# Kernel tuning notes

Hardware: AMD Instinct MI355X
Metric: run time of the kernel (lower is better)

## Reference

```python
import jax, jax.numpy as jnp
import numpy as np

B, T, NU, NX, NY = 16, 4096, 64, 256, 32

def setup_inputs() -> dict:
    key = jax.random.key(0)
    ks = jax.random.split(key, 7)
    s = 1.0 / np.sqrt(NX)
    return {
        "inputs": jax.random.normal(ks[0], (B, T, NU), dtype=jnp.float32),
        "h0": jax.random.uniform(ks[1], (B, NX), dtype=jnp.float32),
        "H_w": jax.random.normal(ks[2], (NX, NX), dtype=jnp.float32) * s,
        "H_b": jax.random.normal(ks[3], (NX,), dtype=jnp.float32) * s,
        "K_w": jax.random.normal(ks[4], (NX, NU), dtype=jnp.float32) * (1.0 / np.sqrt(NU)),
        "E_inv": jnp.eye(NX, dtype=jnp.float32),  # E = I in the original module
        "out_w": jax.random.normal(ks[5], (NY, NX), dtype=jnp.float32) * s,
        "out_b": jax.random.normal(ks[6], (NY,), dtype=jnp.float32) * s,
    }

def reference(inputs, h0, H_w, H_b, K_w, E_inv, out_w, out_b):
    # Precompute input projections for all steps: [B, T, NX]
    Ku = jnp.einsum("btu,xu->btx", inputs, K_w)
    seq_len = inputs.shape[1]

    def step(ht, ku_t):
        xt = ht @ H_w.T + H_b + ku_t          # Linear(H) + Linear(K)
        ht_new = jax.nn.relu(xt) @ E_inv      # nonlinearity then fixed matrix
        return ht_new, ht_new

    # loop runs seq_len - 1 times; states start with h0
    _, hs = jax.lax.scan(step, h0, jnp.swapaxes(Ku[:, : seq_len - 1, :], 0, 1))
    states = jnp.concatenate([h0[:, None, :], jnp.swapaxes(hs, 0, 1)], axis=1)  # [B, T, NX]
    yest = states @ out_w.T + out_b  # [B, T, NY]
    return (yest, states)
```

## Files before the change

### kernel.cpp

```cpp
#include <hip/hip_runtime.h>

#define Bsz 16
#define Tl  4096
#define NUc 64
#define NXc 256
#define NYc 32

template <int CTRL>
__device__ __forceinline__ float dpp_add(float x) {
    int y = __builtin_amdgcn_update_dpp(0, __float_as_int(x), CTRL, 0xf, 0xf, true);
    return x + __int_as_float(y);
}
__device__ __forceinline__ float quad_reduce4(float x) {
    x = dpp_add<0x4E>(x);
    x = dpp_add<0xB1>(x);
    return x;
}
__device__ __forceinline__ float row_reduce16(float x) {
    x = dpp_add<0x128>(x);
    x = dpp_add<0x124>(x);
    x = dpp_add<0x4E>(x);
    x = dpp_add<0xB1>(x);
    return x;
}

#define KEEPF(x) asm volatile("" : "+v"(x))

#define DECLW(T,P) \
    float T##P##_0,T##P##_1,T##P##_2,T##P##_3,T##P##_4,T##P##_5,T##P##_6,T##P##_7, \
          T##P##_8,T##P##_9,T##P##_10,T##P##_11,T##P##_12,T##P##_13,T##P##_14,T##P##_15
#define LOADW(T,P,RP) { \
    const float* wr_ = (RP) + 16*P; \
    float4 a_=*(const float4*)(wr_+0), b_=*(const float4*)(wr_+4); \
    float4 c_=*(const float4*)(wr_+8), d_=*(const float4*)(wr_+12); \
    T##P##_0 =a_.x; T##P##_1 =a_.y; T##P##_2 =a_.z; T##P##_3 =a_.w; \
    T##P##_4 =b_.x; T##P##_5 =b_.y; T##P##_6 =b_.z; T##P##_7 =b_.w; \
    T##P##_8 =c_.x; T##P##_9 =c_.y; T##P##_10=c_.z; T##P##_11=c_.w; \
    T##P##_12=d_.x; T##P##_13=d_.y; T##P##_14=d_.z; T##P##_15=d_.w; }
#define PINW(T,P) \
    KEEPF(T##P##_0);  KEEPF(T##P##_1);  KEEPF(T##P##_2);  KEEPF(T##P##_3);  \
    KEEPF(T##P##_4);  KEEPF(T##P##_5);  KEEPF(T##P##_6);  KEEPF(T##P##_7);  \
    KEEPF(T##P##_8);  KEEPF(T##P##_9);  KEEPF(T##P##_10); KEEPF(T##P##_11); \
    KEEPF(T##P##_12); KEEPF(T##P##_13); KEEPF(T##P##_14); KEEPF(T##P##_15)
#define FMAW(T,P,AC0,AC1) \
    AC0=fmaf(T##P##_0, hv0, AC0); AC1=fmaf(T##P##_1, hv1, AC1); \
    AC0=fmaf(T##P##_2, hv2, AC0); AC1=fmaf(T##P##_3, hv3, AC1); \
    AC0=fmaf(T##P##_4, hv4, AC0); AC1=fmaf(T##P##_5, hv5, AC1); \
    AC0=fmaf(T##P##_6, hv6, AC0); AC1=fmaf(T##P##_7, hv7, AC1); \
    AC0=fmaf(T##P##_8, hv8, AC0); AC1=fmaf(T##P##_9, hv9, AC1); \
    AC0=fmaf(T##P##_10,hv10,AC0); AC1=fmaf(T##P##_11,hv11,AC1); \
    AC0=fmaf(T##P##_12,hv12,AC0); AC1=fmaf(T##P##_13,hv13,AC1); \
    AC0=fmaf(T##P##_14,hv14,AC0); AC1=fmaf(T##P##_15,hv15,AC1)

#define CHUNK(P, O0, O1, O2, O3) { \
    float4 q0_ = *(const float4*)(rb + O0); \
    float4 q1_ = *(const float4*)(rb + O1); \
    float4 q2_ = *(const float4*)(rb + O2); \
    float4 q3_ = *(const float4*)(rb + O3); \
    float hv0=q0_.x, hv1=q0_.y, hv2 =q0_.z, hv3 =q0_.w; \
    float hv4=q1_.x, hv5=q1_.y, hv6 =q1_.z, hv7 =q1_.w; \
    float hv8=q2_.x, hv9=q2_.y, hv10=q2_.z, hv11=q2_.w; \
    float hv12=q3_.x,hv13=q3_.y,hv14=q3_.z, hv15=q3_.w; \
    FMAW(A,P,a0,a1); FMAW(B,P,b0,b1); }

#define KDECL4(Q)  float k##Q##_0, k##Q##_1, k##Q##_2, k##Q##_3
#define KLOAD4(Q) { float4 v_ = *(const float4*)(wr_ + 4*Q); \
    k##Q##_0 = v_.x; k##Q##_1 = v_.y; k##Q##_2 = v_.z; k##Q##_3 = v_.w; }
#define KPIN4(Q)   KEEPF(k##Q##_0); KEEPF(k##Q##_1); KEEPF(k##Q##_2); KEEPF(k##Q##_3)
#define KACC4(Q, U) { \
    s0_ = fmaf(k##Q##_0, (U).x, s0_); s1_ = fmaf(k##Q##_1, (U).y, s1_); \
    s0_ = fmaf(k##Q##_2, (U).z, s0_); s1_ = fmaf(k##Q##_3, (U).w, s1_); }

__global__ __launch_bounds__(256) void ku_kernel(const float* __restrict__ inputs,
                                                 const float* __restrict__ Kw,
                                                 float* __restrict__ Ku) {
    const int x    = threadIdx.x;
    const int row0 = blockIdx.x * 64;

    const float* wr_ = Kw + (size_t)x * NUc;
    KDECL4(0);  KDECL4(1);  KDECL4(2);  KDECL4(3);
    KDECL4(4);  KDECL4(5);  KDECL4(6);  KDECL4(7);
    KDECL4(8);  KDECL4(9);  KDECL4(10); KDECL4(11);
    KDECL4(12); KDECL4(13); KDECL4(14); KDECL4(15);
    KLOAD4(0);  KLOAD4(1);  KLOAD4(2);  KLOAD4(3);
    KLOAD4(4);  KLOAD4(5);  KLOAD4(6);  KLOAD4(7);
    KLOAD4(8);  KLOAD4(9);  KLOAD4(10); KLOAD4(11);
    KLOAD4(12); KLOAD4(13); KLOAD4(14); KLOAD4(15);
    KPIN4(0);  KPIN4(1);  KPIN4(2);  KPIN4(3);
    KPIN4(4);  KPIN4(5);  KPIN4(6);  KPIN4(7);
    KPIN4(8);  KPIN4(9);  KPIN4(10); KPIN4(11);
    KPIN4(12); KPIN4(13); KPIN4(14); KPIN4(15);

    __shared__ float sin_[64 * NUc];
    {
        const float* src = inputs + (size_t)row0 * NUc;
        #pragma unroll
        for (int i = 0; i < 16; ++i)
            sin_[threadIdx.x + i * 256] = src[threadIdx.x + i * 256];
    }
    __syncthreads();

    for (int r = 0; r < 64; ++r) {
        const float4* hp = (const float4*)(&sin_[r * NUc]);
        float s0_ = 0.f, s1_ = 0.f;
        KACC4(0,  hp[0]);  KACC4(1,  hp[1]);  KACC4(2,  hp[2]);  KACC4(3,  hp[3]);
        KACC4(4,  hp[4]);  KACC4(5,  hp[5]);  KACC4(6,  hp[6]);  KACC4(7,  hp[7]);
        KACC4(8,  hp[8]);  KACC4(9,  hp[9]);  KACC4(10, hp[10]); KACC4(11, hp[11]);
        KACC4(12, hp[12]); KACC4(13, hp[13]); KACC4(14, hp[14]); KACC4(15, hp[15]);
        Ku[(size_t)(row0 + r) * NXc + x] = s0_ + s1_;
    }
}

template <bool USE_KU>
__global__ __attribute__((amdgpu_flat_work_group_size(512, 512),
                          amdgpu_waves_per_eu(2, 2)))
void scan3(const float* __restrict__ Ku,
           const float* __restrict__ inputs,
           const float* __restrict__ Kw,
           const float* __restrict__ h0,
           const float* __restrict__ Hw,
           const float* __restrict__ Hb,
           float* __restrict__ states) {
    const int b   = blockIdx.x;
    const int tid = threadIdx.x;
    const int c   = tid & 3;
    const int jg  = tid >> 2;
    const int rA  = 2 * jg;
    const int rB  = rA + 1;
    const int row_w = rA + (c & 1);

    __shared__ __align__(16) char shmem[4096];
    float* shf = (float*)shmem;

    DECLW(A,0); DECLW(A,1); DECLW(A,2); DECLW(A,3);
    DECLW(B,0); DECLW(B,1); DECLW(B,2); DECLW(B,3);
    {
        const float* pA = Hw + (size_t)rA * NXc + 64 * c;
        const float* pB = Hw + (size_t)rB * NXc + 64 * c;
        LOADW(A,0,pA); LOADW(A,1,pA); LOADW(A,2,pA); LOADW(A,3,pA);
        LOADW(B,0,pB); LOADW(B,1,pB); LOADW(B,2,pB); LOADW(B,3,pB);
    }
    DECLW(KA,0); DECLW(KB,0);
    if (!USE_KU) {
        const float* qA = Kw + (size_t)rA * NUc + 16 * c;
        const float* qB = Kw + (size_t)rB * NUc + 16 * c;
        LOADW(KA,0,qA); LOADW(KB,0,qB);
    }

    const float bias = Hb[row_w];

    const int wr_pos  = row_w + 4 * (row_w >> 5);
    int wr_off = 2048 + 4 * wr_pos;
    int rd_off = 288 * c;

    const float* kub = Ku + (size_t)b * Tl * NXc;
    const float* inb = inputs + (size_t)b * Tl * NUc + 16 * c;
    float*       stb = states + (size_t)b * Tl * NXc;

    float kuv = 0.f;
    int   ku_idx = row_w;
    float uc0,uc1,uc2,uc3,uc4,uc5,uc6,uc7,uc8,uc9,uc10,uc11,uc12,uc13,uc14,uc15;
    if (USE_KU) {
        kuv = kub[ku_idx];
    } else {
        float4 A_=*(const float4*)(inb+0), B_=*(const float4*)(inb+4);
        float4 C_=*(const float4*)(inb+8), D_=*(const float4*)(inb+12);
        uc0=A_.x;uc1=A_.y;uc2=A_.z;uc3=A_.w; uc4=B_.x;uc5=B_.y;uc6=B_.z;uc7=B_.w;
        uc8=C_.x;uc9=C_.y;uc10=C_.z;uc11=C_.w;uc12=D_.x;uc13=D_.y;uc14=D_.z;uc15=D_.w;
    }

    int st_idx = row_w;
    {
        float h = h0[b * NXc + row_w];
        shf[wr_pos] = h;
        stb[st_idx] = h;
    }
    __syncthreads();

    for (int t = 0; t < Tl - 1; ++t) {
        PINW(A,0); PINW(A,1); PINW(A,2); PINW(A,3);
        PINW(B,0); PINW(B,1); PINW(B,2); PINW(B,3);
        if (!USE_KU) { PINW(KA,0); PINW(KB,0); }

        const char* rb = (const char*)shmem + rd_off;

        float ku_nxt = 0.f;
        float4 un0, un1, un2, un3;
        if (USE_KU) {
            ku_idx += NXc;
            ku_nxt = kub[ku_idx];
        } else {
            int tn = t + 1; if (tn > Tl - 2) tn = Tl - 2;
            const float* up = inb + (size_t)tn * NUc;
            un0 = *(const float4*)(up+0); un1 = *(const float4*)(up+4);
            un2 = *(const float4*)(up+8); un3 = *(const float4*)(up+12);
        }

        float a0 = 0.f, a1 = 0.f, b0 = 0.f, b1 = 0.f;
        CHUNK(0,   0,  16,  32,  48);
        CHUNK(1,  64,  80,  96, 112);
        CHUNK(2, 144, 160, 176, 192);
        CHUNK(3, 208, 224, 240, 256);
        if (!USE_KU) {
            { float hv0=uc0,hv1=uc1,hv2=uc2,hv3=uc3,hv4=uc4,hv5=uc5,hv6=uc6,hv7=uc7,
                    hv8=uc8,hv9=uc9,hv10=uc10,hv11=uc11,hv12=uc12,hv13=uc13,hv14=uc14,hv15=uc15;
              FMAW(KA,0,a0,a1); FMAW(KB,0,b0,b1); }
        }

        float sumA = quad_reduce4(a0 + a1);
        float sumB = quad_reduce4(b0 + b1);

        float v = (c & 1) ? sumB : sumA;
        float s = v + bias + (USE_KU ? kuv : 0.f);
        float h = s > 0.f ? s : 0.f;

        *(float*)((char*)shmem + wr_off) = h;
        st_idx += NXc;
        stb[st_idx] = h;

        if (USE_KU) {
            kuv = ku_nxt;
        } else {
            uc0=un0.x;uc1=un0.y;uc2=un0.z;uc3=un0.w; uc4=un1.x;uc5=un1.y;uc6=un1.z;uc7=un1.w;
            uc8=un2.x;uc9=un2.y;uc10=un2.z;uc11=un2.w;uc12=un3.x;uc13=un3.y;uc14=un3.z;uc15=un3.w;
        }
        __syncthreads();
        rd_off ^= 2048;
        wr_off ^= 2048;
    }
}

__global__ __launch_bounds__(512, 2) void yest2(const float* __restrict__ states,
                                                const float* __restrict__ ow,
                                                const float* __restrict__ obv,
                                                float* __restrict__ yest) {
    const int tid = threadIdx.x;
    const int c   = tid & 15;
    const int g   = tid >> 4;

    float y0_,y1_,y2_,y3_,y4_,y5_,y6_,y7_,y8_,y9_,y10_,y11_,y12_,y13_,y14_,y15_;
    {
        const float* wr = ow + (size_t)g * NXc + 16 * c;
        float4 vA = *(const float4*)(wr + 0),  vB = *(const float4*)(wr + 4);
        float4 vC = *(const float4*)(wr + 8),  vD = *(const float4*)(wr + 12);
        y0_=vA.x; y1_=vA.y; y2_ =vA.z; y3_ =vA.w;
        y4_=vB.x; y5_=vB.y; y6_ =vB.z; y7_ =vB.w;
        y8_=vC.x; y9_=vC.y; y10_=vC.z; y11_=vC.w;
        y12_=vD.x;y13_=vD.y;y14_=vD.z; y15_=vD.w;
        KEEPF(y0_); KEEPF(y1_); KEEPF(y2_);  KEEPF(y3_);
        KEEPF(y4_); KEEPF(y5_); KEEPF(y6_);  KEEPF(y7_);
        KEEPF(y8_); KEEPF(y9_); KEEPF(y10_); KEEPF(y11_);
        KEEPF(y12_);KEEPF(y13_);KEEPF(y14_); KEEPF(y15_);
    }
    const float ob = obv[g];

    const int row0 = blockIdx.x * 256;
    for (int r = 0; r < 256; r += 2) {
        const float* s0p = states + (size_t)(row0 + r) * NXc + 16 * c;
        const float* s1p = s0p + NXc;
        float4 A0 = *(const float4*)(s0p + 0), A1 = *(const float4*)(s0p + 4);
        float4 A2 = *(const float4*)(s0p + 8), A3 = *(const float4*)(s0p + 12);
        float4 B0 = *(const float4*)(s1p + 0), B1 = *(const float4*)(s1p + 4);
        float4 B2 = *(const float4*)(s1p + 8), B3 = *(const float4*)(s1p + 12);
        float acc0 = y0_*A0.x + y1_*A0.y + y2_*A0.z + y3_*A0.w
                   + y4_*A1.x + y5_*A1.y + y6_*A1.z + y7_*A1.w
                   + y8_*A2.x + y9_*A2.y + y10_*A2.z + y11_*A2.w
                   + y12_*A3.x + y13_*A3.y + y14_*A3.z + y15_*A3.w;
        float acc1 = y0_*B0.x + y1_*B0.y + y2_*B0.z + y3_*B0.w
                   + y4_*B1.x + y5_*B1.y + y6_*B1.z + y7_*B1.w
                   + y8_*B2.x + y9_*B2.y + y10_*B2.z + y11_*B2.w
                   + y12_*B3.x + y13_*B3.y + y14_*B3.z + y15_*B3.w;
        acc0 = row_reduce16(acc0);
        acc1 = row_reduce16(acc1);
        if (c == 0) {
            yest[(size_t)(row0 + r)     * NYc + g] = acc0 + ob;
            yest[(size_t)(row0 + r + 1) * NYc + g] = acc1 + ob;
        }
    }
}

extern "C" void kernel_launch(void* const* d_in, const int* in_sizes, int n_in,
                              void* d_out, int out_size, void* d_ws, size_t ws_size,
                              hipStream_t stream) {
    const float* inputs = (const float*)d_in[0];
    const float* h0     = (const float*)d_in[1];
    const float* Hw     = (const float*)d_in[2];
    const float* Hb     = (const float*)d_in[3];
    const float* Kw     = (const float*)d_in[4];
    const float* ow     = (const float*)d_in[6];
    const float* ob     = (const float*)d_in[7];

    float* yest   = (float*)d_out;
    float* states = (float*)d_out + (size_t)Bsz * Tl * NYc;

    const size_t ku_bytes = (size_t)Bsz * Tl * NXc * sizeof(float);
    const int    nrows    = Bsz * Tl;

    if (ws_size >= ku_bytes) {
        float* Ku = (float*)d_ws;
        ku_kernel<<<dim3(nrows / 64), dim3(256), 0, stream>>>(inputs, Kw, Ku);
        scan3<true><<<dim3(Bsz), dim3(512), 0, stream>>>(Ku, inputs, Kw, h0, Hw, Hb, states);
    } else {
        scan3<false><<<dim3(Bsz), dim3(512), 0, stream>>>(nullptr, inputs, Kw, h0, Hw, Hb, states);
    }
    yest2<<<dim3(nrows / 256), dim3(512), 0, stream>>>(states, ow, ob, yest);
}
```

Baseline: 2.231 ms.

## Split scan matvec across 8 lanes per 4 rows, lighter barrier

The recurrent scan now has each group of 8 lanes compute 4 output rows, each lane covering 32 columns, instead of 4 lanes computing 2 rows over 64 columns. This halves the serial FMA chain per step at the cost of a 3-step DPP reduction spanning 8 lanes. __syncthreads is replaced by a raw s_waitcnt lgkmcnt(0) plus s_barrier to cut per-step sync overhead. The output projection kernel processes half as many rows per block to launch more blocks.

```diff
diff --git a/kernel.cpp b/kernel.cpp
--- a/kernel.cpp
+++ b/kernel.cpp
@@ -11,9 +11,10 @@
     int y = __builtin_amdgcn_update_dpp(0, __float_as_int(x), CTRL, 0xf, 0xf, true);
     return x + __int_as_float(y);
 }
-__device__ __forceinline__ float quad_reduce4(float x) {
+__device__ __forceinline__ float reduce8(float x) {
+    x = dpp_add<0xB1>(x);
     x = dpp_add<0x4E>(x);
-    x = dpp_add<0xB1>(x);
+    x = dpp_add<0x141>(x);
     return x;
 }
 __device__ __forceinline__ float row_reduce16(float x) {
@@ -22,6 +23,10 @@
     x = dpp_add<0x4E>(x);
     x = dpp_add<0xB1>(x);
     return x;
+}
+
+__device__ __forceinline__ void fast_barrier() {
+    asm volatile("s_waitcnt lgkmcnt(0)\n\ts_barrier" ::: "memory");
 }
 
 #define KEEPF(x) asm volatile("" : "+v"(x))
@@ -52,7 +57,7 @@
     AC0=fmaf(T##P##_12,hv12,AC0); AC1=fmaf(T##P##_13,hv13,AC1); \
     AC0=fmaf(T##P##_14,hv14,AC0); AC1=fmaf(T##P##_15,hv15,AC1)
 
-#define CHUNK(P, O0, O1, O2, O3) { \
+#define CHUNK4(P, O0, O1, O2, O3) { \
     float4 q0_ = *(const float4*)(rb + O0); \
     float4 q1_ = *(const float4*)(rb + O1); \
     float4 q2_ = *(const float4*)(rb + O2); \
@@ -61,7 +66,22 @@
     float hv4=q1_.x, hv5=q1_.y, hv6 =q1_.z, hv7 =q1_.w; \
     float hv8=q2_.x, hv9=q2_.y, hv10=q2_.z, hv11=q2_.w; \
     float hv12=q3_.x,hv13=q3_.y,hv14=q3_.z, hv15=q3_.w; \
-    FMAW(A,P,a0,a1); FMAW(B,P,b0,b1); }
+    FMAW(A,P,aA0,aA1); FMAW(B,P,aB0,aB1); \
+    FMAW(C,P,aC0,aC1); FMAW(D,P,aD0,aD1); }
+
+#define DECLK8(T) float kk##T##_0,kk##T##_1,kk##T##_2,kk##T##_3,kk##T##_4,kk##T##_5,kk##T##_6,kk##T##_7
+#define LOADK8(T,RP) { \
+    float4 a_=*(const float4*)(RP), b_=*(const float4*)((RP)+4); \
+    kk##T##_0=a_.x; kk##T##_1=a_.y; kk##T##_2=a_.z; kk##T##_3=a_.w; \
+    kk##T##_4=b_.x; kk##T##_5=b_.y; kk##T##_6=b_.z; kk##T##_7=b_.w; }
+#define PINK8(T) \
+    KEEPF(kk##T##_0); KEEPF(kk##T##_1); KEEPF(kk##T##_2); KEEPF(kk##T##_3); \
+    KEEPF(kk##T##_4); KEEPF(kk##T##_5); KEEPF(kk##T##_6); KEEPF(kk##T##_7)
+#define FMAK8(T,AC0,AC1) \
+    AC0=fmaf(kk##T##_0,uu0,AC0); AC1=fmaf(kk##T##_1,uu1,AC1); \
+    AC0=fmaf(kk##T##_2,uu2,AC0); AC1=fmaf(kk##T##_3,uu3,AC1); \
+    AC0=fmaf(kk##T##_4,uu4,AC0); AC1=fmaf(kk##T##_5,uu5,AC1); \
+    AC0=fmaf(kk##T##_6,uu6,AC0); AC1=fmaf(kk##T##_7,uu7,AC1)
 
 #define KDECL4(Q)  float k##Q##_0, k##Q##_1, k##Q##_2, k##Q##_3
 #define KLOAD4(Q) { float4 v_ = *(const float4*)(wr_ + 4*Q); \
@@ -114,7 +134,7 @@
 template <bool USE_KU>
 __global__ __attribute__((amdgpu_flat_work_group_size(512, 512),
                           amdgpu_waves_per_eu(2, 2)))
-void scan3(const float* __restrict__ Ku,
+void scan4(const float* __restrict__ Ku,
            const float* __restrict__ inputs,
            const float* __restrict__ Kw,
            const float* __restrict__ h0,
@@ -123,50 +143,48 @@
            float* __restrict__ states) {
     const int b   = blockIdx.x;
     const int tid = threadIdx.x;
-    const int c   = tid & 3;
-    const int jg  = tid >> 2;
-    const int rA  = 2 * jg;
-    const int rB  = rA + 1;
-    const int row_w = rA + (c & 1);
+    const int c   = tid & 7;
+    const int jg  = tid >> 3;
+    const int r0  = 4 * jg;
+    const int row_w = r0 + (c & 3);
 
     __shared__ __align__(16) char shmem[4096];
     float* shf = (float*)shmem;
 
-    DECLW(A,0); DECLW(A,1); DECLW(A,2); DECLW(A,3);
-    DECLW(B,0); DECLW(B,1); DECLW(B,2); DECLW(B,3);
+    DECLW(A,0); DECLW(A,1); DECLW(B,0); DECLW(B,1);
+    DECLW(C,0); DECLW(C,1); DECLW(D,0); DECLW(D,1);
     {
-        const float* pA = Hw + (size_t)rA * NXc + 64 * c;
-        const float* pB = Hw + (size_t)rB * NXc + 64 * c;
-        LOADW(A,0,pA); LOADW(A,1,pA); LOADW(A,2,pA); LOADW(A,3,pA);
-        LOADW(B,0,pB); LOADW(B,1,pB); LOADW(B,2,pB); LOADW(B,3,pB);
-    }
-    DECLW(KA,0); DECLW(KB,0);
+        const float* p = Hw + (size_t)r0 * NXc + 32 * c;
+        LOADW(A,0,p); LOADW(A,1,p);  p += NXc;
+        LOADW(B,0,p); LOADW(B,1,p);  p += NXc;
+        LOADW(C,0,p); LOADW(C,1,p);  p += NXc;
+        LOADW(D,0,p); LOADW(D,1,p);
+    }
+    DECLK8(A); DECLK8(B); DECLK8(C); DECLK8(D);
     if (!USE_KU) {
-        const float* qA = Kw + (size_t)rA * NUc + 16 * c;
-        const float* qB = Kw + (size_t)rB * NUc + 16 * c;
-        LOADW(KA,0,qA); LOADW(KB,0,qB);
+        const float* q = Kw + (size_t)r0 * NUc + 8 * c;
+        LOADK8(A,q); q += NUc; LOADK8(B,q); q += NUc;
+        LOADK8(C,q); q += NUc; LOADK8(D,q);
     }
 
     const float bias = Hb[row_w];
 
-    const int wr_pos  = row_w + 4 * (row_w >> 5);
+    const int wr_pos = row_w + 4 * (row_w >> 5);
     int wr_off = 2048 + 4 * wr_pos;
-    int rd_off = 288 * c;
+    int rd_off = 144 * c;
 
     const float* kub = Ku + (size_t)b * Tl * NXc;
-    const float* inb = inputs + (size_t)b * Tl * NUc + 16 * c;
+    const float* inb = inputs + (size_t)b * Tl * NUc + 8 * c;
     float*       stb = states + (size_t)b * Tl * NXc;
 
     float kuv = 0.f;
-    int   ku_idx = row_w;
-    float uc0,uc1,uc2,uc3,uc4,uc5,uc6,uc7,uc8,uc9,uc10,uc11,uc12,uc13,uc14,uc15;
+    float uu0,uu1,uu2,uu3,uu4,uu5,uu6,uu7;
     if (USE_KU) {
-        kuv = kub[ku_idx];
+        kuv = kub[row_w];
     } else {
-        float4 A_=*(const float4*)(inb+0), B_=*(const float4*)(inb+4);
-        float4 C_=*(const float4*)(inb+8), D_=*(const float4*)(inb+12);
-        uc0=A_.x;uc1=A_.y;uc2=A_.z;uc3=A_.w; uc4=B_.x;uc5=B_.y;uc6=B_.z;uc7=B_.w;
-        uc8=C_.x;uc9=C_.y;uc10=C_.z;uc11=C_.w;uc12=D_.x;uc13=D_.y;uc14=D_.z;uc15=D_.w;
+        float4 a_ = *(const float4*)(inb + 0), b_ = *(const float4*)(inb + 4);
+        uu0=a_.x; uu1=a_.y; uu2=a_.z; uu3=a_.w;
+        uu4=b_.x; uu5=b_.y; uu6=b_.z; uu7=b_.w;
     }
 
     int st_idx = row_w;
@@ -178,39 +196,38 @@
     __syncthreads();
 
     for (int t = 0; t < Tl - 1; ++t) {
-        PINW(A,0); PINW(A,1); PINW(A,2); PINW(A,3);
-        PINW(B,0); PINW(B,1); PINW(B,2); PINW(B,3);
-        if (!USE_KU) { PINW(KA,0); PINW(KB,0); }
+        PINW(A,0); PINW(A,1); PINW(B,0); PINW(B,1);
+        PINW(C,0); PINW(C,1); PINW(D,0); PINW(D,1);
+        if (!USE_KU) { PINK8(A); PINK8(B); PINK8(C); PINK8(D); }
 
         const char* rb = (const char*)shmem + rd_off;
 
         float ku_nxt = 0.f;
-        float4 un0, un1, un2, un3;
+        float4 un0, un1;
         if (USE_KU) {
-            ku_idx += NXc;
-            ku_nxt = kub[ku_idx];
+            ku_nxt = kub[(size_t)(t + 1) * NXc + row_w];
         } else {
             int tn = t + 1; if (tn > Tl - 2) tn = Tl - 2;
             const float* up = inb + (size_t)tn * NUc;
-            un0 = *(const float4*)(up+0); un1 = *(const float4*)(up+4);
-            un2 = *(const float4*)(up+8); un3 = *(const float4*)(up+12);
+            un0 = *(const float4*)(up + 0); un1 = *(const float4*)(up + 4);
         }
 
-        float a0 = 0.f, a1 = 0.f, b0 = 0.f, b1 = 0.f;
-        CHUNK(0,   0,  16,  32,  48);
-        CHUNK(1,  64,  80,  96, 112);
-        CHUNK(2, 144, 160, 176, 192);
-        CHUNK(3, 208, 224, 240, 256);
+        float aA0=0.f,aA1=0.f,aB0=0.f,aB1=0.f,aC0=0.f,aC1=0.f,aD0=0.f,aD1=0.f;
+        CHUNK4(0,  0, 16, 32, 48);
+        CHUNK4(1, 64, 80, 96, 112);
         if (!USE_KU) {
-            { float hv0=uc0,hv1=uc1,hv2=uc2,hv3=uc3,hv4=uc4,hv5=uc5,hv6=uc6,hv7=uc7,
-                    hv8=uc8,hv9=uc9,hv10=uc10,hv11=uc11,hv12=uc12,hv13=uc13,hv14=uc14,hv15=uc15;
-              FMAW(KA,0,a0,a1); FMAW(KB,0,b0,b1); }
+            FMAK8(A,aA0,aA1); FMAK8(B,aB0,aB1);
+            FMAK8(C,aC0,aC1); FMAK8(D,aD0,aD1);
         }
 
-        float sumA = quad_reduce4(a0 + a1);
-        float sumB = quad_reduce4(b0 + b1);
-
-        float v = (c & 1) ? sumB : sumA;
+        float sA = reduce8(aA0 + aA1);
+        float sB = reduce8(aB0 + aB1);
+        float sC = reduce8(aC0 + aC1);
+        float sD = reduce8(aD0 + aD1);
+
+        float x = (c & 1) ? sB : sA;
+        float y = (c & 1) ? sD : sC;
+        float v = (c & 2) ? y : x;
         float s = v + bias + (USE_KU ? kuv : 0.f);
         float h = s > 0.f ? s : 0.f;
 
@@ -221,10 +238,10 @@
         if (USE_KU) {
             kuv = ku_nxt;
         } else {
-            uc0=un0.x;uc1=un0.y;uc2=un0.z;uc3=un0.w; uc4=un1.x;uc5=un1.y;uc6=un1.z;uc7=un1.w;
-            uc8=un2.x;uc9=un2.y;uc10=un2.z;uc11=un2.w;uc12=un3.x;uc13=un3.y;uc14=un3.z;uc15=un3.w;
+            uu0=un0.x; uu1=un0.y; uu2=un0.z; uu3=un0.w;
+            uu4=un1.x; uu5=un1.y; uu6=un1.z; uu7=un1.w;
         }
-        __syncthreads();
+        fast_barrier();
         rd_off ^= 2048;
         wr_off ^= 2048;
     }
@@ -254,8 +271,8 @@
     }
     const float ob = obv[g];
 
-    const int row0 = blockIdx.x * 256;
-    for (int r = 0; r < 256; r += 2) {
+    const int row0 = blockIdx.x * 128;
+    for (int r = 0; r < 128; r += 2) {
         const float* s0p = states + (size_t)(row0 + r) * NXc + 16 * c;
         const float* s1p = s0p + NXc;
         float4 A0 = *(const float4*)(s0p + 0), A1 = *(const float4*)(s0p + 4);
@@ -299,9 +316,9 @@
     if (ws_size >= ku_bytes) {
         float* Ku = (float*)d_ws;
         ku_kernel<<<dim3(nrows / 64), dim3(256), 0, stream>>>(inputs, Kw, Ku);
-        scan3<true><<<dim3(Bsz), dim3(512), 0, stream>>>(Ku, inputs, Kw, h0, Hw, Hb, states);
+        scan4<true><<<dim3(Bsz), dim3(512), 0, stream>>>(Ku, inputs, Kw, h0, Hw, Hb, states);
     } else {
-        scan3<false><<<dim3(Bsz), dim3(512), 0, stream>>>(nullptr, inputs, Kw, h0, Hw, Hb, states);
-    }
-    yest2<<<dim3(nrows / 256), dim3(512), 0, stream>>>(states, ow, ob, yest);
-}
+        scan4<false><<<dim3(Bsz), dim3(512), 0, stream>>>(nullptr, inputs, Kw, h0, Hw, Hb, states);
+    }
+    yest2<<<dim3(nrows / 128), dim3(512), 0, stream>>>(states, ow, ob, yest);
+}
```

Measured after the change: 2.055 ms. 7.9% less time.
